# Kernel optimization log

Measured on AMD Instinct MI355X. Metric: run time of the kernel, lower is better.

Reference implementation:

```python
import jax, jax.numpy as jnp
import numpy as np

N_NODES = 100000
K_HOPS = 3  # PyG TAGConv default


def _gcn_norm(edge_index, num_nodes):
    # Symmetric normalization WITHOUT self-loops (TAGConv default).
    row, col = edge_index[0], edge_index[1]
    ones = jnp.ones(row.shape[0], dtype=jnp.float32)
    deg = jax.ops.segment_sum(ones, col, num_segments=num_nodes)
    dinv = jnp.where(deg > 0, jax.lax.rsqrt(jnp.maximum(deg, 1.0)), 0.0)
    return dinv[row] * dinv[col]


def _tagconv(x, row, col, norm, W, b, num_nodes):
    # out = Linear(concat_{k=0..K} (D^-1/2 A D^-1/2)^k x)
    xs = [x]
    h = x
    for _ in range(K_HOPS):
        h = jax.ops.segment_sum(norm[:, None] * h[row], col, num_segments=num_nodes)
        xs.append(h)
    return jnp.concatenate(xs, axis=-1) @ W.T + b


def setup_inputs() -> dict:
    key = jax.random.key(0)
    k1, k2, k3, k4, k5 = jax.random.split(key, 5)
    in_c, hid_c, out_c = 128, 128, 128
    n_edges = 1600000
    x = jax.random.normal(k1, (N_NODES, in_c), dtype=jnp.float32)
    edge_index = jax.random.randint(k2, (2, n_edges), 0, N_NODES, dtype=jnp.int64)
    s1 = 1.0 / np.sqrt(in_c * (K_HOPS + 1))
    s2 = 1.0 / np.sqrt(hid_c * (K_HOPS + 1))
    W1 = jax.random.normal(k3, (hid_c, in_c * (K_HOPS + 1)), dtype=jnp.float32) * s1
    b1 = jnp.zeros((hid_c,), dtype=jnp.float32)
    W2 = jax.random.normal(k4, (out_c, hid_c * (K_HOPS + 1)), dtype=jnp.float32) * s2
    b2 = jnp.zeros((out_c,), dtype=jnp.float32)
    return {"x": x, "edge_index": edge_index, "W1": W1, "b1": b1, "W2": W2, "b2": b2}


def reference(x, edge_index, W1, b1, W2, b2):
    row, col = edge_index[0], edge_index[1]
    norm = _gcn_norm(edge_index, N_NODES)  # [E]
    h = jax.nn.relu(_tagconv(x, row, col, norm, W1, b1, N_NODES))
    out = _tagconv(h, row, col, norm, W2, b2, N_NODES)
    return out.reshape(-1)  # original: x.view(n_nodes * out_channels)
```

## Files before the change

kernel.cpp:

```cpp
#include <hip/hip_runtime.h>
#include <hip/hip_fp16.h>

#define FEAT 128
#define SCAN_CHUNK 1024

typedef _Float16 half_t;
typedef _Float16 half4 __attribute__((ext_vector_type(4)));
typedef _Float16 half8 __attribute__((ext_vector_type(8)));
typedef float float4v __attribute__((ext_vector_type(4)));

__global__ void count_kernel(const int* __restrict__ col, int* __restrict__ deg, int E) {
    int e = blockIdx.x * blockDim.x + threadIdx.x;
    if (e < E) atomicAdd(&deg[col[e]], 1);
}

__global__ __launch_bounds__(256) void scan_partial_kernel(const int* __restrict__ deg,
                                                           int* __restrict__ partials, int n) {
    __shared__ int sd[256];
    int base = blockIdx.x * SCAN_CHUNK;
    int t = threadIdx.x;
    int s = 0;
#pragma unroll
    for (int j = 0; j < 4; ++j) {
        int i = base + t + j * 256;
        if (i < n) s += deg[i];
    }
    sd[t] = s;
    __syncthreads();
    for (int o = 128; o > 0; o >>= 1) {
        if (t < o) sd[t] += sd[t + o];
        __syncthreads();
    }
    if (t == 0) partials[blockIdx.x] = sd[0];
}

__global__ __launch_bounds__(1024) void scan_top_kernel(int* __restrict__ partials, int nb,
                                                        int* __restrict__ totalp) {
    __shared__ int sd[1024];
    int t = threadIdx.x;
    int v = (t < nb) ? partials[t] : 0;
    sd[t] = v;
    __syncthreads();
    for (int o = 1; o < 1024; o <<= 1) {
        int u = (t >= o) ? sd[t - o] : 0;
        __syncthreads();
        sd[t] += u;
        __syncthreads();
    }
    if (t < nb) partials[t] = sd[t] - v;
    if (t == nb - 1) *totalp = sd[t];
}

__global__ __launch_bounds__(256) void scan_final_kernel(const int* __restrict__ deg,
                                                         const int* __restrict__ partials,
                                                         int* __restrict__ offs,
                                                         float* __restrict__ dinv, int n) {
    __shared__ int sums[256];
    __shared__ int blockoff;
    int base = blockIdx.x * SCAN_CHUNK;
    int t = threadIdx.x;
    int v[4];
    int s = 0;
#pragma unroll
    for (int j = 0; j < 4; ++j) {
        int i = base + 4 * t + j;
        v[j] = (i < n) ? deg[i] : 0;
        s += v[j];
    }
    sums[t] = s;
    if (t == 0) blockoff = partials[blockIdx.x];
    __syncthreads();
    int mine = s;
    for (int o = 1; o < 256; o <<= 1) {
        int u = (t >= o) ? sums[t - o] : 0;
        __syncthreads();
        sums[t] += u;
        __syncthreads();
    }
    int ex = sums[t] - mine + blockoff;
#pragma unroll
    for (int j = 0; j < 4; ++j) {
        int i = base + 4 * t + j;
        if (i < n) {
            offs[i] = ex;
            dinv[i] = (v[j] > 0) ? rsqrtf((float)v[j]) : 0.0f;
        }
        ex += v[j];
    }
}

__global__ void fill_kernel(const int* __restrict__ row, const int* __restrict__ col,
                            const float* __restrict__ dinv,
                            int* __restrict__ cursor,
                            int2* __restrict__ csr, int E) {
    int e = blockIdx.x * blockDim.x + threadIdx.x;
    if (e < E) {
        int r = row[e];
        int c = col[e];
        int pos = atomicAdd(&cursor[c], 1);
        float w = dinv[r] * dinv[c];
        int2 pk;
        pk.x = r;
        pk.y = __float_as_int(w);
        csr[pos] = pk;
    }
}

__global__ void f2h3_kernel(const float* __restrict__ a, half_t* __restrict__ ah, int na4,
                            const float* __restrict__ b, half_t* __restrict__ bh, int nb4,
                            const float* __restrict__ c, half_t* __restrict__ ch, int nc4) {
    int i = blockIdx.x * blockDim.x + threadIdx.x;
    const float* src;
    half_t* dst;
    int j = i;
    if (j < na4) { src = a; dst = ah; }
    else if ((j -= na4) < nb4) { src = b; dst = bh; }
    else if ((j -= nb4) < nc4) { src = c; dst = ch; }
    else return;
    float4 v = ((const float4*)src)[j];
    half4 o;
    o.x = (half_t)v.x; o.y = (half_t)v.y; o.z = (half_t)v.z; o.w = (half_t)v.w;
    ((half4*)dst)[j] = o;
}

__global__ __launch_bounds__(256) void prop16_kernel(const half_t* __restrict__ src,
                                                     half_t* __restrict__ dst,
                                                     const int* __restrict__ offs,
                                                     const int2* __restrict__ csr, int N) {
    int v = blockIdx.x * 8 + (threadIdx.x >> 5);
    if (v >= N) return;
    int lane = threadIdx.x & 31;
    int s0 = offs[v];
    int s1 = offs[v + 1];
    float4v a0 = (float4v)0.0f, a1 = (float4v)0.0f, a2 = (float4v)0.0f, a3 = (float4v)0.0f;
    int i = s0;
    for (; i + 3 < s1; i += 4) {
        int2 e0 = csr[i], e1 = csr[i + 1], e2 = csr[i + 2], e3 = csr[i + 3];
        half4 v0 = *(const half4*)(src + (size_t)e0.x * FEAT + lane * 4);
        half4 v1 = *(const half4*)(src + (size_t)e1.x * FEAT + lane * 4);
        half4 v2 = *(const half4*)(src + (size_t)e2.x * FEAT + lane * 4);
        half4 v3 = *(const half4*)(src + (size_t)e3.x * FEAT + lane * 4);
        float w0 = __int_as_float(e0.y), w1 = __int_as_float(e1.y);
        float w2 = __int_as_float(e2.y), w3 = __int_as_float(e3.y);
        a0.x = fmaf(w0, (float)v0.x, a0.x); a0.y = fmaf(w0, (float)v0.y, a0.y);
        a0.z = fmaf(w0, (float)v0.z, a0.z); a0.w = fmaf(w0, (float)v0.w, a0.w);
        a1.x = fmaf(w1, (float)v1.x, a1.x); a1.y = fmaf(w1, (float)v1.y, a1.y);
        a1.z = fmaf(w1, (float)v1.z, a1.z); a1.w = fmaf(w1, (float)v1.w, a1.w);
        a2.x = fmaf(w2, (float)v2.x, a2.x); a2.y = fmaf(w2, (float)v2.y, a2.y);
        a2.z = fmaf(w2, (float)v2.z, a2.z); a2.w = fmaf(w2, (float)v2.w, a2.w);
        a3.x = fmaf(w3, (float)v3.x, a3.x); a3.y = fmaf(w3, (float)v3.y, a3.y);
        a3.z = fmaf(w3, (float)v3.z, a3.z); a3.w = fmaf(w3, (float)v3.w, a3.w);
    }
    for (; i < s1; ++i) {
        int2 e0 = csr[i];
        float w0 = __int_as_float(e0.y);
        half4 v0 = *(const half4*)(src + (size_t)e0.x * FEAT + lane * 4);
        a0.x = fmaf(w0, (float)v0.x, a0.x); a0.y = fmaf(w0, (float)v0.y, a0.y);
        a0.z = fmaf(w0, (float)v0.z, a0.z); a0.w = fmaf(w0, (float)v0.w, a0.w);
    }
    half4 o;
    o.x = (half_t)((a0.x + a1.x) + (a2.x + a3.x));
    o.y = (half_t)((a0.y + a1.y) + (a2.y + a3.y));
    o.z = (half_t)((a0.z + a1.z) + (a2.z + a3.z));
    o.w = (half_t)((a0.w + a1.w) + (a2.w + a3.w));
    *(half4*)(dst + (size_t)v * FEAT + lane * 4) = o;
}

template <bool RELU, bool HALFOUT>
__global__ __launch_bounds__(256) void gemm16_kernel(const half_t* __restrict__ H0,
                                                     const half_t* __restrict__ H1,
                                                     const half_t* __restrict__ H2,
                                                     const half_t* __restrict__ H3,
                                                     const half_t* __restrict__ W,
                                                     const float* __restrict__ bias,
                                                     half_t* __restrict__ out_h,
                                                     float* __restrict__ out_f, int N) {
    __shared__ half_t ws[128][40];
    const int tid = threadIdx.x;
    const int lane = tid & 63;
    const int wid = tid >> 6;
    const int lr = lane & 15;
    const int lk = lane >> 4;
    const int m = blockIdx.x * 64 + wid * 16 + lr;
    const bool mok = (m < N);

    float4v acc[8];
#pragma unroll
    for (int ct = 0; ct < 8; ++ct) acc[ct] = (float4v)0.0f;

    const half_t* Hs[4] = {H0, H1, H2, H3};
    const int wo = tid >> 1;
    const int wh = tid & 1;

#pragma unroll
    for (int b = 0; b < 4; ++b) {
        const half_t* __restrict__ H = Hs[b];
#pragma unroll
        for (int kt = 0; kt < 128; kt += 32) {
            half8 hfrag = (half8)(half_t)0.0f;
            if (mok) hfrag = *(const half8*)(H + (size_t)m * FEAT + kt + lk * 8);
            const half8* wsrc = (const half8*)(W + (size_t)wo * 512 + b * 128 + kt + wh * 16);
            half8 w0 = wsrc[0];
            half8 w1 = wsrc[1];
            __syncthreads();
            *(half8*)&ws[wo][wh * 16 + 0] = w0;
            *(half8*)&ws[wo][wh * 16 + 8] = w1;
            __syncthreads();
#pragma unroll
            for (int ct = 0; ct < 8; ++ct) {
                half8 wfrag = *(const half8*)&ws[ct * 16 + lr][lk * 8];
                acc[ct] = __builtin_amdgcn_mfma_f32_16x16x32_f16(wfrag, hfrag, acc[ct], 0, 0, 0);
            }
        }
    }

    if (mok) {
#pragma unroll
        for (int ct = 0; ct < 8; ++ct) {
            int o = ct * 16 + lk * 4;
            float4 bv = *(const float4*)(bias + o);
            float r0 = acc[ct][0] + bv.x;
            float r1 = acc[ct][1] + bv.y;
            float r2 = acc[ct][2] + bv.z;
            float r3 = acc[ct][3] + bv.w;
            if (RELU) {
                r0 = fmaxf(r0, 0.0f); r1 = fmaxf(r1, 0.0f);
                r2 = fmaxf(r2, 0.0f); r3 = fmaxf(r3, 0.0f);
            }
            if (HALFOUT) {
                half4 hv;
                hv.x = (half_t)r0; hv.y = (half_t)r1; hv.z = (half_t)r2; hv.w = (half_t)r3;
                *(half4*)(out_h + (size_t)m * FEAT + o) = hv;
            } else {
                float4 fv;
                fv.x = r0; fv.y = r1; fv.z = r2; fv.w = r3;
                *(float4*)(out_f + (size_t)m * FEAT + o) = fv;
            }
        }
    }
}

extern "C" void kernel_launch(void* const* d_in, const int* in_sizes, int n_in,
                              void* d_out, int out_size, void* d_ws, size_t ws_size,
                              hipStream_t stream) {
    const float* x   = (const float*)d_in[0];
    const int*   ei  = (const int*)d_in[1];
    const float* W1  = (const float*)d_in[2];
    const float* b1  = (const float*)d_in[3];
    const float* W2  = (const float*)d_in[4];
    const float* b2  = (const float*)d_in[5];
    float* out = (float*)d_out;

    const int N = in_sizes[0] / FEAT;
    const int E = in_sizes[1] / 2;
    const int* row = ei;
    const int* col = ei + E;
    const int nb = (N + SCAN_CHUNK - 1) / SCAN_CHUNK;

    size_t off = 0;
    auto carve = [&](size_t bytes) -> void* {
        void* p = (char*)d_ws + off;
        off += (bytes + 255) & ~(size_t)255;
        return p;
    };
    int*    deg      = (int*)carve((size_t)N * 4);
    int*    cursor   = (int*)carve((size_t)N * 4);
    float*  dinv     = (float*)carve((size_t)N * 4);
    int*    offs     = (int*)carve((size_t)(N + 1) * 4);
    int*    partials = (int*)carve((size_t)nb * 4);
    int2*   csr      = (int2*)carve((size_t)E * 8);
    half_t* x16      = (half_t*)carve((size_t)N * FEAT * 2);
    half_t* t1       = (half_t*)carve((size_t)N * FEAT * 2);
    half_t* t2       = (half_t*)carve((size_t)N * FEAT * 2);
    half_t* t3       = (half_t*)carve((size_t)N * FEAT * 2);
    half_t* hbuf     = (half_t*)carve((size_t)N * FEAT * 2);
    half_t* w1h      = (half_t*)carve((size_t)FEAT * 512 * 2);
    half_t* w2h      = (half_t*)carve((size_t)FEAT * 512 * 2);

    const int tB = 256;
    const int gE = (E + tB - 1) / tB;
    const int gP = (N + 7) / 8;
    const int gG = (N + 63) / 64;
    const int xt4 = N * FEAT / 4;
    const int wt4 = FEAT * 512 / 4;
    const int cvt_total = xt4 + 2 * wt4;

    hipMemsetAsync(deg, 0, (size_t)N * 4, stream);
    count_kernel<<<gE, tB, 0, stream>>>(col, deg, E);
    scan_partial_kernel<<<nb, 256, 0, stream>>>(deg, partials, N);
    scan_top_kernel<<<1, 1024, 0, stream>>>(partials, nb, offs + N);
    scan_final_kernel<<<nb, 256, 0, stream>>>(deg, partials, offs, dinv, N);
    hipMemcpyAsync(cursor, offs, (size_t)N * 4, hipMemcpyDeviceToDevice, stream);
    fill_kernel<<<gE, tB, 0, stream>>>(row, col, dinv, cursor, csr, E);

    f2h3_kernel<<<(cvt_total + tB - 1) / tB, tB, 0, stream>>>(x, x16, xt4, W1, w1h, wt4, W2, w2h, wt4);

    prop16_kernel<<<gP, 256, 0, stream>>>(x16, t1, offs, csr, N);
    prop16_kernel<<<gP, 256, 0, stream>>>(t1, t2, offs, csr, N);
    prop16_kernel<<<gP, 256, 0, stream>>>(t2, t3, offs, csr, N);
    gemm16_kernel<true, true><<<gG, 256, 0, stream>>>(x16, t1, t2, t3, w1h, b1, hbuf, nullptr, N);

    prop16_kernel<<<gP, 256, 0, stream>>>(hbuf, t1, offs, csr, N);
    prop16_kernel<<<gP, 256, 0, stream>>>(t1, t2, offs, csr, N);
    prop16_kernel<<<gP, 256, 0, stream>>>(t2, t3, offs, csr, N);
    gemm16_kernel<false, false><<<gG, 256, 0, stream>>>(hbuf, t1, t2, t3, w2h, b2, nullptr, out, N);
}
```

Measured before the change: 617.4 us.

## Build CSR via two-pass bucketed scatter with shared-memory atomics

Replaces the single-pass CSR fill, which used global atomics on per-node cursors and scattered writes, with two passes. The first pass scatters edges into 128-node buckets using far fewer global atomic counters. The second pass does a per-bucket fill with LDS atomics and writes the normalized weights. It also adds nontemporal loads for the edge streams and CSR reads in propagation, at the cost of an extra temp buffer and an extra pass over the edges.

```diff
diff --git a/kernel.cpp b/kernel.cpp
--- a/kernel.cpp
+++ b/kernel.cpp
@@ -3,6 +3,8 @@
 
 #define FEAT 128
 #define SCAN_CHUNK 1024
+#define BSZ 128
+#define BSH 7
 
 typedef _Float16 half_t;
 typedef _Float16 half4 __attribute__((ext_vector_type(4)));
@@ -11,7 +13,10 @@
 
 __global__ void count_kernel(const int* __restrict__ col, int* __restrict__ deg, int E) {
     int e = blockIdx.x * blockDim.x + threadIdx.x;
-    if (e < E) atomicAdd(&deg[col[e]], 1);
+    if (e < E) {
+        int c = __builtin_nontemporal_load(col + e);
+        atomicAdd(&deg[c], 1);
+    }
 }
 
 __global__ __launch_bounds__(256) void scan_partial_kernel(const int* __restrict__ deg,
@@ -89,20 +94,50 @@
     }
 }
 
-__global__ void fill_kernel(const int* __restrict__ row, const int* __restrict__ col,
-                            const float* __restrict__ dinv,
-                            int* __restrict__ cursor,
-                            int2* __restrict__ csr, int E) {
+__global__ void binit_kernel(const int* __restrict__ offs, int* __restrict__ bcur, int NB) {
+    int b = blockIdx.x * blockDim.x + threadIdx.x;
+    if (b < NB) bcur[b] = offs[b << BSH];
+}
+
+__global__ void bucketA_kernel(const int* __restrict__ row, const int* __restrict__ col,
+                               int* __restrict__ bcur, int2* __restrict__ tmp, int E) {
     int e = blockIdx.x * blockDim.x + threadIdx.x;
     if (e < E) {
-        int r = row[e];
-        int c = col[e];
-        int pos = atomicAdd(&cursor[c], 1);
-        float w = dinv[r] * dinv[c];
+        int r = __builtin_nontemporal_load(row + e);
+        int c = __builtin_nontemporal_load(col + e);
+        int b = c >> BSH;
+        int pos = atomicAdd(&bcur[b], 1);
         int2 pk;
         pk.x = r;
-        pk.y = __float_as_int(w);
-        csr[pos] = pk;
+        pk.y = c;
+        tmp[pos] = pk;
+    }
+}
+
+__global__ __launch_bounds__(256) void bfill_kernel(const int2* __restrict__ tmp,
+                                                    const int* __restrict__ offs,
+                                                    const float* __restrict__ dinv,
+                                                    int2* __restrict__ csr, int N) {
+    __shared__ int lcur[BSZ];
+    int b = blockIdx.x;
+    int lo = b << BSH;
+    int hi = lo + BSZ;
+    if (hi > N) hi = N;
+    int t = threadIdx.x;
+    if (t < hi - lo) lcur[t] = offs[lo + t];
+    __syncthreads();
+    int base = offs[lo];
+    int end = offs[hi];
+    for (int i = base + t; i < end; i += 256) {
+        long long pk = __builtin_nontemporal_load((const long long*)(tmp + i));
+        int r = (int)(pk & 0xffffffffLL);
+        int c = (int)(pk >> 32);
+        int pos = atomicAdd(&lcur[c - lo], 1);
+        float w = dinv[r] * dinv[c];
+        int2 o;
+        o.x = r;
+        o.y = __float_as_int(w);
+        csr[pos] = o;
     }
 }
 
@@ -135,13 +170,18 @@
     float4v a0 = (float4v)0.0f, a1 = (float4v)0.0f, a2 = (float4v)0.0f, a3 = (float4v)0.0f;
     int i = s0;
     for (; i + 3 < s1; i += 4) {
-        int2 e0 = csr[i], e1 = csr[i + 1], e2 = csr[i + 2], e3 = csr[i + 3];
-        half4 v0 = *(const half4*)(src + (size_t)e0.x * FEAT + lane * 4);
-        half4 v1 = *(const half4*)(src + (size_t)e1.x * FEAT + lane * 4);
-        half4 v2 = *(const half4*)(src + (size_t)e2.x * FEAT + lane * 4);
-        half4 v3 = *(const half4*)(src + (size_t)e3.x * FEAT + lane * 4);
-        float w0 = __int_as_float(e0.y), w1 = __int_as_float(e1.y);
-        float w2 = __int_as_float(e2.y), w3 = __int_as_float(e3.y);
+        long long p0 = __builtin_nontemporal_load((const long long*)(csr + i));
+        long long p1 = __builtin_nontemporal_load((const long long*)(csr + i + 1));
+        long long p2 = __builtin_nontemporal_load((const long long*)(csr + i + 2));
+        long long p3 = __builtin_nontemporal_load((const long long*)(csr + i + 3));
+        int r0 = (int)(p0 & 0xffffffffLL), r1 = (int)(p1 & 0xffffffffLL);
+        int r2 = (int)(p2 & 0xffffffffLL), r3 = (int)(p3 & 0xffffffffLL);
+        half4 v0 = *(const half4*)(src + (size_t)r0 * FEAT + lane * 4);
+        half4 v1 = *(const half4*)(src + (size_t)r1 * FEAT + lane * 4);
+        half4 v2 = *(const half4*)(src + (size_t)r2 * FEAT + lane * 4);
+        half4 v3 = *(const half4*)(src + (size_t)r3 * FEAT + lane * 4);
+        float w0 = __int_as_float((int)(p0 >> 32)), w1 = __int_as_float((int)(p1 >> 32));
+        float w2 = __int_as_float((int)(p2 >> 32)), w3 = __int_as_float((int)(p3 >> 32));
         a0.x = fmaf(w0, (float)v0.x, a0.x); a0.y = fmaf(w0, (float)v0.y, a0.y);
         a0.z = fmaf(w0, (float)v0.z, a0.z); a0.w = fmaf(w0, (float)v0.w, a0.w);
         a1.x = fmaf(w1, (float)v1.x, a1.x); a1.y = fmaf(w1, (float)v1.y, a1.y);
@@ -152,9 +192,10 @@
         a3.z = fmaf(w3, (float)v3.z, a3.z); a3.w = fmaf(w3, (float)v3.w, a3.w);
     }
     for (; i < s1; ++i) {
-        int2 e0 = csr[i];
-        float w0 = __int_as_float(e0.y);
-        half4 v0 = *(const half4*)(src + (size_t)e0.x * FEAT + lane * 4);
+        long long p0 = __builtin_nontemporal_load((const long long*)(csr + i));
+        int r0 = (int)(p0 & 0xffffffffLL);
+        float w0 = __int_as_float((int)(p0 >> 32));
+        half4 v0 = *(const half4*)(src + (size_t)r0 * FEAT + lane * 4);
         a0.x = fmaf(w0, (float)v0.x, a0.x); a0.y = fmaf(w0, (float)v0.y, a0.y);
         a0.z = fmaf(w0, (float)v0.z, a0.z); a0.w = fmaf(w0, (float)v0.w, a0.w);
     }
@@ -256,6 +297,7 @@
     const int* row = ei;
     const int* col = ei + E;
     const int nb = (N + SCAN_CHUNK - 1) / SCAN_CHUNK;
+    const int NB = (N + BSZ - 1) / BSZ;
 
     size_t off = 0;
     auto carve = [&](size_t bytes) -> void* {
@@ -264,10 +306,11 @@
         return p;
     };
     int*    deg      = (int*)carve((size_t)N * 4);
-    int*    cursor   = (int*)carve((size_t)N * 4);
     float*  dinv     = (float*)carve((size_t)N * 4);
     int*    offs     = (int*)carve((size_t)(N + 1) * 4);
     int*    partials = (int*)carve((size_t)nb * 4);
+    int*    bcur     = (int*)carve((size_t)NB * 4);
+    int2*   tmp      = (int2*)carve((size_t)E * 8);
     int2*   csr      = (int2*)carve((size_t)E * 8);
     half_t* x16      = (half_t*)carve((size_t)N * FEAT * 2);
     half_t* t1       = (half_t*)carve((size_t)N * FEAT * 2);
@@ -290,8 +333,9 @@
     scan_partial_kernel<<<nb, 256, 0, stream>>>(deg, partials, N);
     scan_top_kernel<<<1, 1024, 0, stream>>>(partials, nb, offs + N);
     scan_final_kernel<<<nb, 256, 0, stream>>>(deg, partials, offs, dinv, N);
-    hipMemcpyAsync(cursor, offs, (size_t)N * 4, hipMemcpyDeviceToDevice, stream);
-    fill_kernel<<<gE, tB, 0, stream>>>(row, col, dinv, cursor, csr, E);
+    binit_kernel<<<(NB + tB - 1) / tB, tB, 0, stream>>>(offs, bcur, NB);
+    bucketA_kernel<<<gE, tB, 0, stream>>>(row, col, bcur, tmp, E);
+    bfill_kernel<<<NB, 256, 0, stream>>>(tmp, offs, dinv, csr, N);
 
     f2h3_kernel<<<(cvt_total + tB - 1) / tB, tB, 0, stream>>>(x, x16, xt4, W1, w1h, wt4, W2, w2h, wt4);
 
```

Result: slower. 993.3 us (+60.9%).
